# Optimization experiments

Hardware: AMD Instinct MI355X
Metric: run time of the kernel (lower is better)

## Reference

```python
import jax, jax.numpy as jnp
import numpy as np

DIM = 512
HEADS = 8
DIM_HEAD = 64
INNER = HEADS * DIM_HEAD          # 512
CPB_DIM = DIM // 2                # 256 (ContinuousPositionBias hidden dim)
FF_INNER = int(DIM * 4 * 2 / 3)   # 1365 (GEGLU inner dim)
B, C, F, H, W = 2, 512, 8, 32, 32
SCALE = DIM_HEAD ** -0.5


def setup_inputs() -> dict:
    key = jax.random.key(0)
    ks = jax.random.split(key, 24)
    def rnd(k, shape, s=0.02):
        return jax.random.normal(k, shape, jnp.float32) * s
    return {
        "x": jax.random.normal(ks[0], (B, C, F, W, W), jnp.float32)[:, :, :, :H, :],
        # spatial attention
        "sa_gamma": jnp.ones((DIM,), jnp.float32),
        "sa_wq": rnd(ks[1], (DIM, INNER)),
        "sa_wkv": rnd(ks[2], (DIM, 2 * INNER)),
        "sa_wo": rnd(ks[3], (INNER, DIM)),
        # temporal attention
        "ta_gamma": jnp.ones((DIM,), jnp.float32),
        "ta_wq": rnd(ks[4], (DIM, INNER)),
        "ta_wkv": rnd(ks[5], (DIM, 2 * INNER)),
        "ta_wo": rnd(ks[6], (INNER, DIM)),
        # spatial ContinuousPositionBias MLP (num_dims=2, layers=2)
        "sp_w1": rnd(ks[7], (2, CPB_DIM), 0.1), "sp_b1": jnp.zeros((CPB_DIM,), jnp.float32),
        "sp_w2": rnd(ks[8], (CPB_DIM, CPB_DIM), 0.05), "sp_b2": jnp.zeros((CPB_DIM,), jnp.float32),
        "sp_w3": rnd(ks[9], (CPB_DIM, HEADS), 0.05), "sp_b3": jnp.zeros((HEADS,), jnp.float32),
        # temporal ContinuousPositionBias MLP (num_dims=1)
        "tp_w1": rnd(ks[10], (1, CPB_DIM), 0.1), "tp_b1": jnp.zeros((CPB_DIM,), jnp.float32),
        "tp_w2": rnd(ks[11], (CPB_DIM, CPB_DIM), 0.05), "tp_b2": jnp.zeros((CPB_DIM,), jnp.float32),
        "tp_w3": rnd(ks[12], (CPB_DIM, HEADS), 0.05), "tp_b3": jnp.zeros((HEADS,), jnp.float32),
        # FeedForward: Conv3d 1x1 (no bias) -> GEGLU -> RMSNorm -> Conv3d 1x1
        "ff_win": rnd(ks[13], (DIM, 2 * FF_INNER)),
        "ff_gamma": jnp.ones((FF_INNER,), jnp.float32),
        "ff_wout": rnd(ks[14], (FF_INNER, DIM)),
    }


def _rms_last(x, g):
    # torch: F.normalize(x, dim=-1) * sqrt(C) * gamma
    nrm = jnp.sqrt(jnp.sum(x * x, axis=-1, keepdims=True))
    return x / jnp.maximum(nrm, 1e-12) * jnp.sqrt(jnp.float32(x.shape[-1])) * g


def _mlp_bias(rel, w1, b1, w2, b2, w3, b3):
    h = jax.nn.silu(rel @ w1 + b1)
    h = jax.nn.silu(h @ w2 + b2)
    return h @ w3 + b3  # [R, heads]


def _cpb_2d(h, w, params):
    ry = jnp.arange(-(h - 1), h, dtype=jnp.float32)
    rx = jnp.arange(-(w - 1), w, dtype=jnp.float32)
    gy, gx = jnp.meshgrid(ry, rx, indexing='ij')
    rel = jnp.stack([gy, gx], -1).reshape(-1, 2)          # [(2h-1)(2w-1), 2]
    tab = _mlp_bias(rel, *params)                          # [R, heads]
    py, px = jnp.meshgrid(jnp.arange(h), jnp.arange(w), indexing='ij')
    pos = jnp.stack([py.reshape(-1), px.reshape(-1)], -1)  # [n, 2]
    d = pos[:, None, :] - pos[None, :, :]                  # [n, n, 2]
    idx = (d[..., 0] + h - 1) * (2 * w - 1) + (d[..., 1] + w - 1)
    return jnp.transpose(tab[idx], (2, 0, 1))              # [heads, n, n]


def _cpb_1d(f, params):
    rel = jnp.arange(-(f - 1), f, dtype=jnp.float32)[:, None]
    tab = _mlp_bias(rel, *params)                          # [2f-1, heads]
    p = jnp.arange(f)
    idx = p[:, None] - p[None, :] + f - 1
    return jnp.transpose(tab[idx], (2, 0, 1))              # [heads, f, f]


def _attn(x, gamma, wq, wkv, wo, bias):
    # x: [b, n, c]; manual softmax(QK^T*scale + bias)V (flash disabled by pos_bias)
    xn = _rms_last(x, gamma)
    q = xn @ wq
    k, v = jnp.split(xn @ wkv, 2, axis=-1)
    b, n, _ = q.shape
    rs = lambda t: t.reshape(b, n, HEADS, DIM_HEAD).transpose(0, 2, 1, 3)
    q, k, v = rs(q), rs(k), rs(v)
    s = jnp.einsum('bhid,bhjd->bhij', q, k) * SCALE + bias[None]
    a = jax.nn.softmax(s, axis=-1)
    o = jnp.einsum('bhij,bhjd->bhid', a, v)
    o = o.transpose(0, 2, 1, 3).reshape(b, n, INNER)
    return o @ wo


def _ff(x, win, gamma, wout):
    # x: [b, f, h, w, c] channel-last; Conv3d 1x1 == channel einsum
    hdn = jnp.einsum('bfhwc,co->bfhwo', x, win)
    a, gate = jnp.split(hdn, 2, axis=-1)
    y = a * jax.nn.gelu(gate, approximate=False)           # GEGLU (torch exact gelu)
    # shift_token: chunk channels, shift second half by +1 frame
    c1 = (FF_INNER + 1) // 2
    t1, t2 = y[..., :c1], y[..., c1:]
    t2 = jnp.pad(t2, ((0, 0), (1, 0), (0, 0), (0, 0), (0, 0)))[:, :-1]
    y = jnp.concatenate([t1, t2], axis=-1)
    yn = _rms_last(y, gamma)                               # RMSNorm over channels
    return jnp.einsum('bfhwi,ic->bfhwc', yn, wout)


def reference(x, sa_gamma, sa_wq, sa_wkv, sa_wo, ta_gamma, ta_wq, ta_wkv, ta_wo,
              sp_w1, sp_b1, sp_w2, sp_b2, sp_w3, sp_b3,
              tp_w1, tp_b1, tp_w2, tp_b2, tp_w3, tp_b3,
              ff_win, ff_gamma, ff_wout):
    b, c, f, h, w = x.shape
    xl = jnp.transpose(x, (0, 2, 3, 4, 1))                 # b f h w c
    # spatial attention over (h w) tokens, batched over (b f)
    xs = xl.reshape(b * f, h * w, c)
    sp_bias = _cpb_2d(h, w, (sp_w1, sp_b1, sp_w2, sp_b2, sp_w3, sp_b3))
    xs = _attn(xs, sa_gamma, sa_wq, sa_wkv, sa_wo, sp_bias) + xs
    xv = xs.reshape(b, f, h, w, c)
    # temporal attention over f tokens, batched over (b h w)
    xt = jnp.transpose(xv, (0, 2, 3, 1, 4)).reshape(b * h * w, f, c)
    tp_bias = _cpb_1d(f, (tp_w1, tp_b1, tp_w2, tp_b2, tp_w3, tp_b3))
    xt = _attn(xt, ta_gamma, ta_wq, ta_wkv, ta_wo, tp_bias) + xt
    xv = jnp.transpose(xt.reshape(b, h, w, f, c), (0, 3, 1, 2, 4))
    # GEGLU feedforward with token shift
    xv = _ff(xv, ff_win, ff_gamma, ff_wout) + xv
    return jnp.transpose(xv, (0, 4, 1, 2, 3))              # b c f h w
```

## Files before the change

### kernel.cpp

```cpp
#include <hip/hip_runtime.h>
#include <cstdint>
#include <cstddef>

typedef __bf16 bf16_t;
typedef __bf16 bf16x8 __attribute__((ext_vector_type(8)));
typedef __bf16 bf16x4 __attribute__((ext_vector_type(4)));
typedef float floatx4 __attribute__((ext_vector_type(4)));

__device__ __forceinline__ float wred_sum(float v) {
#pragma unroll
  for (int off = 32; off > 0; off >>= 1) v += __shfl_xor(v, off);
  return v;
}
__device__ __forceinline__ void async16(const void* g, void* l) {
  __builtin_amdgcn_global_load_lds((const __attribute__((address_space(1))) void*)g,
                                   (__attribute__((address_space(3))) void*)l, 16, 0, 0);
}

template <int MODE>
__global__ __launch_bounds__(256) void st_gemm(
    const bf16_t* __restrict__ A, const bf16_t* __restrict__ B, void* Cp, void* Cp2,
    const float* Res, int M, int N, int K, int lda, int ldb, int ldc, int nb1,
    long long sa1, long long sa2, long long sb1, long long sb2,
    long long sc1, long long sc2) {
  __shared__ bf16_t sA[128 * 32];
  __shared__ bf16_t sB[128 * 32];
  const int z = blockIdx.z;
  const int z1 = z % nb1, z2 = z / nb1;
  A += z1 * sa1 + z2 * sa2;
  B += z1 * sb1 + z2 * sb2;
  const long long coff = z1 * sc1 + z2 * sc2;
  const int tid = threadIdx.x;
  const int bm = blockIdx.x, bn = blockIdx.y;
  const int lane = tid & 63;
  const int wave = tid >> 6;
  const int wm = (wave >> 1) * 64, wn = (wave & 1) * 64;
  const int rowf = lane & 15, kq = (lane >> 4) * 8;

  floatx4 acc[4][4];
#pragma unroll
  for (int i = 0; i < 4; ++i)
#pragma unroll
    for (int j = 0; j < 4; ++j) acc[i][j] = floatx4{0.f, 0.f, 0.f, 0.f};

  for (int kt = 0; kt < K; kt += 32) {
#pragma unroll
    for (int it = 0; it < 2; ++it) {
      int slot = it * 256 + tid;
      int mi = slot >> 2, kc = slot & 3;
      int ar = bm * 128 + mi; if (ar > M - 1) ar = M - 1;
      int br = bn * 128 + mi; if (br > N - 1) br = N - 1;
      async16(A + (size_t)ar * lda + kt + kc * 8, (char*)sA + slot * 16);
      async16(B + (size_t)br * ldb + kt + kc * 8, (char*)sB + slot * 16);
    }
    __syncthreads();
    bf16x8 af[4], bv[4];
#pragma unroll
    for (int i = 0; i < 4; ++i) {
      af[i] = *(const bf16x8*)(sA + (wm + i * 16 + rowf) * 32 + kq);
      bv[i] = *(const bf16x8*)(sB + (wn + i * 16 + rowf) * 32 + kq);
    }
#pragma unroll
    for (int i = 0; i < 4; ++i)
#pragma unroll
      for (int j = 0; j < 4; ++j)
        acc[i][j] = __builtin_amdgcn_mfma_f32_16x16x32_bf16(af[i], bv[j], acc[i][j], 0, 0, 0);
    __syncthreads();
  }

  const int cl = lane & 15;
  const int rowBase = bm * 128 + wm + (lane >> 4) * 4;
  if (MODE == 5) {
    bf16_t* yb = (bf16_t*)Cp;
    const int cg0 = ((bn * 128 + wn) >> 5) * 16;
#pragma unroll
    for (int i = 0; i < 4; ++i) {
#pragma unroll
      for (int p = 0; p < 2; ++p) {
        int c = cg0 + p * 16 + cl;
        if (c >= 1365) continue;
#pragma unroll
        for (int r = 0; r < 4; ++r) {
          int row = rowBase + i * 16 + r;
          if (row >= M) continue;
          float a = acc[i][2 * p][r];
          float gt = acc[i][2 * p + 1][r];
          float y = a * 0.5f * gt * (1.f + erff(gt * 0.70710678f));
          yb[(size_t)row * ldc + c] = (bf16_t)y;
        }
      }
    }
    return;
  }
  const int colBase = bn * 128 + wn + cl;
#pragma unroll
  for (int i = 0; i < 4; ++i) {
#pragma unroll
    for (int j = 0; j < 4; ++j) {
      int col = colBase + j * 16;
      if (col >= N) continue;
#pragma unroll
      for (int r = 0; r < 4; ++r) {
        int row = rowBase + i * 16 + r;
        if (row >= M) continue;
        long long inidx = coff + (long long)row * ldc + col;
        float v = acc[i][j][r];
        if (MODE >= 2) v += Res[inidx];
        if (MODE == 0) { ((float*)Cp)[inidx] = v; }
        else if (MODE == 1) { ((bf16_t*)Cp)[inidx] = (bf16_t)v; }
        else if (MODE == 2) { ((float*)Cp)[inidx] = v; }
        else if (MODE == 3) {
          int orow = (row & ~8191) | ((row & 1023) << 3) | ((row >> 10) & 7);
          ((float*)Cp)[coff + (long long)orow * ldc + col] = v;
        } else if (MODE == 4) {
          int orow = (row & ~8191) | ((row & 7) << 10) | ((row >> 3) & 1023);
          long long oidx = coff + (long long)orow * ldc + col;
          ((float*)Cp)[oidx] = v;
          ((bf16_t*)Cp2)[oidx] = (bf16_t)v;
        }
      }
    }
  }
}

__global__ __launch_bounds__(256) void st_transpose2d(
    const float* __restrict__ in, float* __restrict__ out, int R, int Cc,
    long long inb, long long outb) {
  __shared__ float tile[32][33];
  const int ct = blockIdx.x, rt = blockIdx.y, b = blockIdx.z;
  in += (long long)b * inb;
  out += (long long)b * outb;
  const int tx = threadIdx.x & 31, ty = threadIdx.x >> 5;
#pragma unroll
  for (int k = 0; k < 4; ++k) {
    int r = rt * 32 + ty + k * 8;
    int c = ct * 32 + tx;
    tile[ty + k * 8][tx] = in[(size_t)r * Cc + c];
  }
  __syncthreads();
#pragma unroll
  for (int k = 0; k < 4; ++k) {
    int c = ct * 32 + ty + k * 8;
    int r = rt * 32 + tx;
    out[(size_t)c * R + r] = tile[tx][ty + k * 8];
  }
}

__global__ void st_wtrans(const float* __restrict__ src, bf16_t* __restrict__ dst,
                          int K, int Kpad, int N, int srcld, int coloff, long total) {
  long idx = (long)blockIdx.x * 256 + threadIdx.x;
  if (idx >= total) return;
  int kp = (int)(idx % Kpad);
  int n = (int)(idx / Kpad);
  float v = (kp < K) ? src[(size_t)kp * srcld + coloff + n] : 0.f;
  dst[idx] = (bf16_t)v;
}

__global__ void st_wtrans_geglu(const float* __restrict__ src, bf16_t* __restrict__ dst,
                                long total) {
  long idx = (long)blockIdx.x * 256 + threadIdx.x;
  if (idx >= total) return;
  int kp = (int)(idx & 511);
  int n = (int)(idx >> 9);
  int c = ((n >> 5) << 4) + (n & 15);
  float v = 0.f;
  if (c < 1365) {
    int srccol = c + (((n >> 4) & 1) ? 1365 : 0);
    v = src[(size_t)kp * 2730 + srccol];
  }
  dst[idx] = (bf16_t)v;
}

__global__ __launch_bounds__(256) void st_cpb(
    const float* __restrict__ w1, const float* __restrict__ b1,
    const float* __restrict__ w2, const float* __restrict__ b2,
    const float* __restrict__ w3, const float* __restrict__ b3,
    bf16_t* __restrict__ tab2d, float* __restrict__ tab1d, int two_d) {
  const int pos = blockIdx.x, t = threadIdx.x;
  float r0, r1 = 0.f;
  if (two_d) { r0 = (float)(pos / 63 - 31); r1 = (float)(pos % 63 - 31); }
  else { r0 = (float)(pos - 7); }
  __shared__ float sh[256];
  float h = r0 * w1[t] + (two_d ? r1 * w1[256 + t] : 0.f) + b1[t];
  h = h / (1.f + expf(-h));
  sh[t] = h;
  __syncthreads();
  float h2 = b2[t];
  for (int j = 0; j < 256; ++j) h2 += sh[j] * w2[j * 256 + t];
  h2 = h2 / (1.f + expf(-h2));
  __syncthreads();
  sh[t] = h2;
  __syncthreads();
  if (t < 8) {
    float o = b3[t];
    for (int j = 0; j < 256; ++j) o += sh[j] * w3[j * 8 + t];
    if (two_d) tab2d[t * 4000 + pos] = (bf16_t)(o * 1.4426950408889634f);
    else tab1d[t * 15 + pos] = o;
  }
}

__global__ __launch_bounds__(256) void st_rmsnorm(const float* __restrict__ x,
                                                  const float* __restrict__ gamma,
                                                  bf16_t* __restrict__ y) {
  const int token = blockIdx.x * 4 + (threadIdx.x >> 6);
  const int lane = threadIdx.x & 63;
  const float* xr = x + (size_t)token * 512;
  float v[8];
  float ss = 0.f;
#pragma unroll
  for (int k = 0; k < 8; ++k) { v[k] = xr[k * 64 + lane]; ss += v[k] * v[k]; }
  ss = wred_sum(ss);
  const float r = 22.627416998f / fmaxf(sqrtf(ss), 1e-12f);
  bf16_t* yr = y + (size_t)token * 512;
#pragma unroll
  for (int k = 0; k < 8; ++k) yr[k * 64 + lane] = (bf16_t)(v[k] * r * gamma[k * 64 + lane]);
}

__global__ __launch_bounds__(256) void st_vtrans(const bf16_t* __restrict__ qkv,
                                                 bf16_t* __restrict__ vT) {
  __shared__ float tile[32][33];
  const int jt = blockIdx.x, dt = blockIdx.y, z = blockIdx.z;
  const int bf = z >> 3, h = z & 7;
  const int tx = threadIdx.x & 31, ty = threadIdx.x >> 5;
#pragma unroll
  for (int k = 0; k < 4; ++k) {
    int j = jt * 32 + ty + k * 8;
    int d = dt * 32 + tx;
    tile[ty + k * 8][tx] = (float)qkv[((size_t)(bf * 1024 + j)) * 1536 + 1024 + h * 64 + d];
  }
  __syncthreads();
#pragma unroll
  for (int k = 0; k < 4; ++k) {
    int d = dt * 32 + ty + k * 8;
    int j = jt * 32 + tx;
    vT[((size_t)z * 64 + d) * 1024 + j] = (bf16_t)tile[tx][ty + k * 8];
  }
}

__global__ __launch_bounds__(256, 3) void st_flash(
    const bf16_t* __restrict__ qkv, const bf16_t* __restrict__ vT,
    const bf16_t* __restrict__ tabb, bf16_t* __restrict__ ob) {
  __shared__ __align__(16) bf16_t ldsK[2][64 * 64];
  __shared__ __align__(16) bf16_t ldsV[2][64 * 64];
  __shared__ __align__(16) bf16_t ldsP[4 * 32 * 64];
  __shared__ __align__(16) bf16_t ldsT[2216];
  const int qtile = blockIdx.x;
  const int z = blockIdx.y;
  const int bf = z >> 3, h = z & 7;
  const int tid = threadIdx.x;
  const int lane = tid & 63, wave = tid >> 6;
  const int cl = lane & 15, g = lane >> 4;
  const size_t qkvBase = (size_t)bf * 1024 * 1536 + h * 64;
  const int eoff = (qtile * 252) & ~7;
  const bf16_t* Kp = qkv + qkvBase + 512;
  const bf16_t* Vp = vT + (size_t)z * 65536;

#pragma unroll
  for (int it = 0; it < 4; ++it) {
    int s = it * 256 + tid;
    int row = s >> 3, c = s & 7;
    int cs = c ^ (row & 7);
    async16(qkv + qkvBase + (size_t)(qtile * 128 + row) * 1536 + cs * 8,
            (char*)ldsP + s * 16);
  }
#pragma unroll
  for (int it = 0; it < 2; ++it) {
    int s = it * 256 + tid;
    if (s < 277) async16(tabb + h * 4000 + eoff + s * 8, (char*)ldsT + s * 16);
  }
#pragma unroll
  for (int it = 0; it < 2; ++it) {
    int s = it * 256 + tid;
    int row = s >> 3, c = s & 7;
    int cs = c ^ (row & 7);
    async16(Kp + (size_t)row * 1536 + cs * 8, (char*)ldsK[0] + s * 16);
    async16(Vp + (size_t)row * 1024 + cs * 8, (char*)ldsV[0] + s * 16);
  }
  __syncthreads();
  bf16x8 aq[2][2];
#pragma unroll
  for (int it = 0; it < 2; ++it)
#pragma unroll
    for (int ks = 0; ks < 2; ++ks) {
      int row = wave * 32 + it * 16 + cl;
      int cs = (g + ks * 4) ^ (row & 7);
      aq[it][ks] = *(const bf16x8*)(ldsP + row * 64 + cs * 8);
    }
  __syncthreads();

  int fiB[2];
#pragma unroll
  for (int it = 0; it < 2; ++it) {
    int i = qtile * 128 + wave * 32 + it * 16 + cl;
    fiB[it] = (i >> 5) * 63 + (i & 31) + 1984 - eoff;
  }
  float lsum[2] = {0.f, 0.f};
  floatx4 oacc[4][2];
#pragma unroll
  for (int dt = 0; dt < 4; ++dt)
#pragma unroll
    for (int it = 0; it < 2; ++it) oacc[dt][it] = floatx4{0.f, 0.f, 0.f, 0.f};

  bf16_t* ldsPw = ldsP + wave * (32 * 64);
  const float SC = 0.18033688011112042f;

#pragma unroll 2
  for (int t = 0; t < 16; ++t) {
    const int p = t & 1;
    if (t < 15) {
      const int j1 = (t + 1) * 64;
#pragma unroll
      for (int it = 0; it < 2; ++it) {
        int s = it * 256 + tid;
        int row = s >> 3, c = s & 7;
        int cs = c ^ (row & 7);
        async16(Kp + (size_t)(j1 + row) * 1536 + cs * 8, (char*)ldsK[p ^ 1] + s * 16);
        async16(Vp + (size_t)row * 1024 + j1 + cs * 8, (char*)ldsV[p ^ 1] + s * 16);
      }
    }
    const int j0 = t * 64;
    floatx4 sacc[4][2];
#pragma unroll
    for (int jt = 0; jt < 4; ++jt)
#pragma unroll
      for (int it = 0; it < 2; ++it) sacc[jt][it] = floatx4{0.f, 0.f, 0.f, 0.f};
#pragma unroll
    for (int ks = 0; ks < 2; ++ks) {
#pragma unroll
      for (int jt = 0; jt < 4; ++jt) {
        int row = jt * 16 + cl;
        bf16x8 kf = *(const bf16x8*)(ldsK[p] + row * 64 + (((ks * 4 + g) ^ (row & 7))) * 8);
#pragma unroll
        for (int it = 0; it < 2; ++it)
          sacc[jt][it] = __builtin_amdgcn_mfma_f32_16x16x32_bf16(kf, aq[it][ks], sacc[jt][it], 0, 0, 0);
      }
    }
#pragma unroll
    for (int jt = 0; jt < 4; ++jt) {
      int jb = j0 + jt * 16 + g * 4;
      int fjb = (jb >> 5) * 63 + (jb & 31);
      int gg = jt * 2 + (g >> 1);
#pragma unroll
      for (int it = 0; it < 2; ++it) {
        int idx0 = fiB[it] - fjb;
        float e0 = __builtin_exp2f(sacc[jt][it][0] * SC + (float)ldsT[idx0]);
        float e1 = __builtin_exp2f(sacc[jt][it][1] * SC + (float)ldsT[idx0 - 1]);
        float e2 = __builtin_exp2f(sacc[jt][it][2] * SC + (float)ldsT[idx0 - 2]);
        float e3 = __builtin_exp2f(sacc[jt][it][3] * SC + (float)ldsT[idx0 - 3]);
        lsum[it] += (e0 + e1) + (e2 + e3);
        bf16x4 pv = {(bf16_t)e0, (bf16_t)e1, (bf16_t)e2, (bf16_t)e3};
        int prow = it * 16 + cl;
        *(bf16x4*)((char*)ldsPw + prow * 128 + ((gg ^ (cl & 7)) * 16 + (g & 1) * 8)) = pv;
      }
    }
#pragma unroll
    for (int ks = 0; ks < 2; ++ks) {
      bf16x8 pB[2];
#pragma unroll
      for (int it = 0; it < 2; ++it)
        pB[it] = *(const bf16x8*)((char*)ldsPw + (it * 16 + cl) * 128 +
                                  (((ks * 4 + g) ^ (cl & 7)) * 16));
#pragma unroll
      for (int dt = 0; dt < 4; ++dt) {
        int row = dt * 16 + cl;
        bf16x8 vf = *(const bf16x8*)(ldsV[p] + row * 64 + (((ks * 4 + g) ^ (row & 7))) * 8);
#pragma unroll
        for (int it = 0; it < 2; ++it)
          oacc[dt][it] = __builtin_amdgcn_mfma_f32_16x16x32_bf16(vf, pB[it], oacc[dt][it], 0, 0, 0);
      }
    }
    __syncthreads();
  }
  float inv[2];
#pragma unroll
  for (int it = 0; it < 2; ++it) {
    float s = lsum[it];
    s += __shfl_xor(s, 16);
    s += __shfl_xor(s, 32);
    inv[it] = 1.f / s;
  }
#pragma unroll
  for (int it = 0; it < 2; ++it) {
    int i = qtile * 128 + wave * 32 + it * 16 + cl;
    size_t base = ((size_t)bf * 1024 + i) * 512 + h * 64 + g * 4;
#pragma unroll
    for (int dt = 0; dt < 4; ++dt) {
      bf16x4 ov = {(bf16_t)(oacc[dt][it][0] * inv[it]), (bf16_t)(oacc[dt][it][1] * inv[it]),
                   (bf16_t)(oacc[dt][it][2] * inv[it]), (bf16_t)(oacc[dt][it][3] * inv[it])};
      *(bf16x4*)(ob + base + dt * 16) = ov;
    }
  }
}

__global__ __launch_bounds__(256) void st_tattn2(const bf16_t* __restrict__ qkv,
                                                 const float* __restrict__ tabf,
                                                 bf16_t* __restrict__ o) {
  const int wg = blockIdx.x * 4 + (threadIdx.x >> 6);
  const int bhw = wg >> 3, head = wg & 7;
  const int lane = threadIdx.x & 63;
  const size_t base = (size_t)bhw * 8 * 1536 + head * 64 + lane;
  float q[8], k[8], v[8];
#pragma unroll
  for (int f = 0; f < 8; ++f) {
    q[f] = (float)qkv[base + (size_t)f * 1536];
    k[f] = (float)qkv[base + (size_t)f * 1536 + 512];
    v[f] = (float)qkv[base + (size_t)f * 1536 + 1024];
  }
  float p[64];
#pragma unroll
  for (int i = 0; i < 8; ++i)
#pragma unroll
    for (int j = 0; j < 8; ++j) p[i * 8 + j] = q[i] * k[j];
#pragma unroll
  for (int st = 32; st >= 1; st >>= 1) {
    const bool hi = (lane & st) != 0;
#pragma unroll
    for (int m = 0; m < st; ++m) {
      float give = hi ? p[m] : p[m + st];
      float keep = hi ? p[m + st] : p[m];
      p[m] = keep + __shfl_xor(give, st);
    }
  }
  const int i = lane >> 3, j = lane & 7;
  float e = __expf(p[0] * 0.125f + tabf[head * 15 + i - j + 7]);
  float sm = e;
  sm += __shfl_xor(sm, 1);
  sm += __shfl_xor(sm, 2);
  sm += __shfl_xor(sm, 4);
  const float prob = e / sm;
  float acc[8];
#pragma unroll
  for (int ii = 0; ii < 8; ++ii) acc[ii] = 0.f;
#pragma unroll
  for (int ii = 0; ii < 8; ++ii)
#pragma unroll
    for (int jj = 0; jj < 8; ++jj)
      acc[ii] += __shfl(prob, ii * 8 + jj) * v[jj];
#pragma unroll
  for (int ii = 0; ii < 8; ++ii)
    o[(size_t)(bhw * 8 + ii) * 512 + head * 64 + lane] = (bf16_t)acc[ii];
}

__global__ __launch_bounds__(256) void st_glu(const bf16_t* __restrict__ y,
                                              const float* __restrict__ gamma,
                                              bf16_t* __restrict__ yn) {
  const int t = blockIdx.x;
  const int tid = threadIdx.x;
  const int f = (t >> 10) & 7;
  float yv[6];
  float ss = 0.f;
#pragma unroll
  for (int kk = 0; kk < 6; ++kk) {
    int c = kk * 256 + tid;
    float v = 0.f;
    if (c < 1365) {
      long src = t;
      bool valid = true;
      if (c >= 683) { if (f == 0) valid = false; else src = t - 1024; }
      if (valid) v = (float)y[src * 1365 + c];
    }
    yv[kk] = v;
    ss += v * v;
  }
  __shared__ float red[4];
  ss = wred_sum(ss);
  if ((tid & 63) == 0) red[tid >> 6] = ss;
  __syncthreads();
  ss = red[0] + red[1] + red[2] + red[3];
  const float r = sqrtf(1365.f) / fmaxf(sqrtf(ss), 1e-12f);
#pragma unroll
  for (int kk = 0; kk < 6; ++kk) {
    int c = kk * 256 + tid;
    if (c < 1365) yn[(size_t)t * 1376 + c] = (bf16_t)(yv[kk] * r * gamma[c]);
  }
  if (tid < 11) yn[(size_t)t * 1376 + 1365 + tid] = (bf16_t)0.f;
}

extern "C" void kernel_launch(void* const* d_in, const int* in_sizes, int n_in,
                              void* d_out, int out_size, void* d_ws, size_t ws_size,
                              hipStream_t stream) {
  const float* x        = (const float*)d_in[0];
  const float* sa_gamma = (const float*)d_in[1];
  const float* sa_wq    = (const float*)d_in[2];
  const float* sa_wkv   = (const float*)d_in[3];
  const float* sa_wo    = (const float*)d_in[4];
  const float* ta_gamma = (const float*)d_in[5];
  const float* ta_wq    = (const float*)d_in[6];
  const float* ta_wkv   = (const float*)d_in[7];
  const float* ta_wo    = (const float*)d_in[8];
  const float* sp_w1 = (const float*)d_in[9];
  const float* sp_b1 = (const float*)d_in[10];
  const float* sp_w2 = (const float*)d_in[11];
  const float* sp_b2 = (const float*)d_in[12];
  const float* sp_w3 = (const float*)d_in[13];
  const float* sp_b3 = (const float*)d_in[14];
  const float* tp_w1 = (const float*)d_in[15];
  const float* tp_b1 = (const float*)d_in[16];
  const float* tp_w2 = (const float*)d_in[17];
  const float* tp_b2 = (const float*)d_in[18];
  const float* tp_w3 = (const float*)d_in[19];
  const float* tp_b3 = (const float*)d_in[20];
  const float* ff_win   = (const float*)d_in[21];
  const float* ff_gamma = (const float*)d_in[22];
  const float* ff_wout  = (const float*)d_in[23];
  float* outp = (float*)d_out;

  char* ws = (char*)d_ws;
  size_t off = 0;
  auto alloc = [&](size_t bytes) -> char* {
    char* p = ws + off;
    off += (bytes + 255) & ~(size_t)255;
    return p;
  };
  const long T = 16384;
  float*  xs  = (float*)alloc((size_t)T * 512 * 4);
  bf16_t* xn  = (bf16_t*)alloc((size_t)T * 512 * 2);
  char*   R2  = alloc((size_t)T * 1536 * 2);
  char*   R3  = alloc((size_t)T * 1536 * 2);
  char*   R4  = alloc((size_t)T * 1376 * 2);
  bf16_t* wqkvT_sa = (bf16_t*)alloc(1536ULL * 512 * 2);
  bf16_t* woT_sa   = (bf16_t*)alloc(512ULL * 512 * 2);
  bf16_t* wqkvT_ta = (bf16_t*)alloc(1536ULL * 512 * 2);
  bf16_t* woT_ta   = (bf16_t*)alloc(512ULL * 512 * 2);
  bf16_t* winT  = (bf16_t*)alloc(2752ULL * 512 * 2);
  bf16_t* woutT = (bf16_t*)alloc(512ULL * 1376 * 2);
  bf16_t* tabb  = (bf16_t*)alloc(8 * 4000 * 2);
  float*  tabf  = (float*)alloc(8 * 15 * 4);

  bf16_t* qkv  = (bf16_t*)R2;
  bf16_t* ybuf = (bf16_t*)R2;
  bf16_t* vT   = (bf16_t*)R3;
  float*  xt   = (float*)R3;
  bf16_t* ob_s = xn;
  bf16_t* ob_t = (bf16_t*)R4;
  bf16_t* ynb  = (bf16_t*)R4;

  st_transpose2d<<<dim3(256, 16, 2), 256, 0, stream>>>(x, xs, 512, 8192,
                                                       (long long)512 * 8192, (long long)512 * 8192);
  auto wt = [&](const float* src, bf16_t* dst, int K, int Kpad, int N, int srcld, int coloff) {
    long tot = (long)N * Kpad;
    st_wtrans<<<dim3((tot + 255) / 256), 256, 0, stream>>>(src, dst, K, Kpad, N, srcld, coloff, tot);
  };
  wt(sa_wq, wqkvT_sa, 512, 512, 512, 512, 0);
  wt(sa_wkv, wqkvT_sa + 512 * 512, 512, 512, 1024, 1024, 0);
  wt(sa_wo, woT_sa, 512, 512, 512, 512, 0);
  wt(ta_wq, wqkvT_ta, 512, 512, 512, 512, 0);
  wt(ta_wkv, wqkvT_ta + 512 * 512, 512, 512, 1024, 1024, 0);
  wt(ta_wo, woT_ta, 512, 512, 512, 512, 0);
  st_wtrans_geglu<<<dim3((2752 * 512) / 256), 256, 0, stream>>>(ff_win, winT, 2752L * 512);
  wt(ff_wout, woutT, 1365, 1376, 512, 512, 0);
  st_cpb<<<dim3(3969), 256, 0, stream>>>(sp_w1, sp_b1, sp_w2, sp_b2, sp_w3, sp_b3, tabb, tabf, 1);
  st_cpb<<<dim3(15), 256, 0, stream>>>(tp_w1, tp_b1, tp_w2, tp_b2, tp_w3, tp_b3, tabb, tabf, 0);

  st_rmsnorm<<<dim3(4096), 256, 0, stream>>>(xs, sa_gamma, xn);
  st_gemm<1><<<dim3(128, 12, 1), 256, 0, stream>>>(
      xn, wqkvT_sa, (void*)qkv, nullptr, nullptr, 16384, 1536, 512, 512, 512, 1536, 1, 0, 0, 0, 0, 0, 0);
  st_vtrans<<<dim3(32, 2, 128), 256, 0, stream>>>(qkv, vT);
  st_flash<<<dim3(8, 128), 256, 0, stream>>>(qkv, vT, tabb, ob_s);
  st_gemm<3><<<dim3(128, 4, 1), 256, 0, stream>>>(
      ob_s, woT_sa, (void*)xt, nullptr, xs, 16384, 512, 512, 512, 512, 512, 1, 0, 0, 0, 0, 0, 0);

  st_rmsnorm<<<dim3(4096), 256, 0, stream>>>(xt, ta_gamma, xn);
  st_gemm<1><<<dim3(128, 12, 1), 256, 0, stream>>>(
      xn, wqkvT_ta, (void*)qkv, nullptr, nullptr, 16384, 1536, 512, 512, 512, 1536, 1, 0, 0, 0, 0, 0, 0);
  st_tattn2<<<dim3(4096), 256, 0, stream>>>(qkv, tabf, ob_t);
  st_gemm<4><<<dim3(128, 4, 1), 256, 0, stream>>>(
      ob_t, woT_ta, (void*)xs, (void*)xn, xt, 16384, 512, 512, 512, 512, 512, 1, 0, 0, 0, 0, 0, 0);

  st_gemm<5><<<dim3(128, 22, 1), 256, 0, stream>>>(
      xn, winT, (void*)ybuf, nullptr, nullptr, 16384, 2752, 512, 512, 512, 1365, 1, 0, 0, 0, 0, 0, 0);
  st_glu<<<dim3(16384), 256, 0, stream>>>(ybuf, ff_gamma, ynb);
  st_gemm<2><<<dim3(128, 4, 1), 256, 0, stream>>>(
      ynb, woutT, (void*)xs, nullptr, xs, 16384, 512, 1376, 1376, 1376, 512, 1, 0, 0, 0, 0, 0, 0);

  st_transpose2d<<<dim3(16, 256, 2), 256, 0, stream>>>(xs, outp, 8192, 512,
                                                       (long long)8192 * 512, (long long)8192 * 512);
}
```

Before: 713.2 us.

## Shrink flash KV tile to 32 and fold bias into MFMA accumulator init

The spatial flash kernel now streams K/V in 32-row tiles instead of 64, which shrinks LDS buffers and raises the launch-bounds occupancy target from 3 to 4 blocks per CU. Q fragments are read directly from global memory instead of being staged through LDS. The position-bias table is stored as fp32 prescaled by 8, so it can seed the MFMA accumulator and the separate per-element bias add before exp2 disappears. The trade-off is twice as many loop iterations and barriers per block, and a larger fp32 bias table to load.

```diff
diff --git a/kernel.cpp b/kernel.cpp
--- a/kernel.cpp
+++ b/kernel.cpp
@@ -175,7 +175,7 @@
     const float* __restrict__ w1, const float* __restrict__ b1,
     const float* __restrict__ w2, const float* __restrict__ b2,
     const float* __restrict__ w3, const float* __restrict__ b3,
-    bf16_t* __restrict__ tab2d, float* __restrict__ tab1d, int two_d) {
+    float* __restrict__ tab2d, float* __restrict__ tab1d, int two_d) {
   const int pos = blockIdx.x, t = threadIdx.x;
   float r0, r1 = 0.f;
   if (two_d) { r0 = (float)(pos / 63 - 31); r1 = (float)(pos % 63 - 31); }
@@ -194,7 +194,7 @@
   if (t < 8) {
     float o = b3[t];
     for (int j = 0; j < 256; ++j) o += sh[j] * w3[j * 8 + t];
-    if (two_d) tab2d[t * 4000 + pos] = (bf16_t)(o * 1.4426950408889634f);
+    if (two_d) tab2d[t * 4000 + pos] = o * 8.0f;
     else tab1d[t * 15 + pos] = o;
   }
 }
@@ -237,13 +237,13 @@
   }
 }
 
-__global__ __launch_bounds__(256, 3) void st_flash(
+__global__ __launch_bounds__(256, 4) void st_flash(
     const bf16_t* __restrict__ qkv, const bf16_t* __restrict__ vT,
-    const bf16_t* __restrict__ tabb, bf16_t* __restrict__ ob) {
-  __shared__ __align__(16) bf16_t ldsK[2][64 * 64];
-  __shared__ __align__(16) bf16_t ldsV[2][64 * 64];
-  __shared__ __align__(16) bf16_t ldsP[4 * 32 * 64];
-  __shared__ __align__(16) bf16_t ldsT[2216];
+    const float* __restrict__ tab2f, bf16_t* __restrict__ ob) {
+  __shared__ __align__(16) bf16_t ldsK[2][32 * 64];
+  __shared__ __align__(16) bf16_t ldsV[2][64 * 32];
+  __shared__ __align__(16) bf16_t ldsP[4 * 32 * 32];
+  __shared__ __align__(16) float ldsT[2208];
   const int qtile = blockIdx.x;
   const int z = blockIdx.y;
   const int bf = z >> 3, h = z & 7;
@@ -251,40 +251,28 @@
   const int lane = tid & 63, wave = tid >> 6;
   const int cl = lane & 15, g = lane >> 4;
   const size_t qkvBase = (size_t)bf * 1024 * 1536 + h * 64;
-  const int eoff = (qtile * 252) & ~7;
+  const int eoff = (qtile * 252) & ~3;
   const bf16_t* Kp = qkv + qkvBase + 512;
   const bf16_t* Vp = vT + (size_t)z * 65536;
 
 #pragma unroll
-  for (int it = 0; it < 4; ++it) {
+  for (int it = 0; it < 3; ++it) {
     int s = it * 256 + tid;
-    int row = s >> 3, c = s & 7;
-    int cs = c ^ (row & 7);
-    async16(qkv + qkvBase + (size_t)(qtile * 128 + row) * 1536 + cs * 8,
-            (char*)ldsP + s * 16);
-  }
-#pragma unroll
-  for (int it = 0; it < 2; ++it) {
-    int s = it * 256 + tid;
-    if (s < 277) async16(tabb + h * 4000 + eoff + s * 8, (char*)ldsT + s * 16);
-  }
-#pragma unroll
-  for (int it = 0; it < 2; ++it) {
-    int s = it * 256 + tid;
-    int row = s >> 3, c = s & 7;
-    int cs = c ^ (row & 7);
-    async16(Kp + (size_t)row * 1536 + cs * 8, (char*)ldsK[0] + s * 16);
-    async16(Vp + (size_t)row * 1024 + cs * 8, (char*)ldsV[0] + s * 16);
-  }
-  __syncthreads();
+    if (s < 552) async16(tab2f + h * 4000 + eoff + s * 4, (char*)ldsT + s * 16);
+  }
+  {
+    int row = tid >> 3, c = tid & 7, cs = c ^ (row & 7);
+    async16(Kp + (size_t)row * 1536 + cs * 8, (char*)ldsK[0] + tid * 16);
+    int rv = tid >> 2, cv = tid & 3, csv = cv ^ (rv & 3);
+    async16(Vp + (size_t)rv * 1024 + csv * 8, (char*)ldsV[0] + tid * 16);
+  }
   bf16x8 aq[2][2];
 #pragma unroll
   for (int it = 0; it < 2; ++it)
 #pragma unroll
     for (int ks = 0; ks < 2; ++ks) {
-      int row = wave * 32 + it * 16 + cl;
-      int cs = (g + ks * 4) ^ (row & 7);
-      aq[it][ks] = *(const bf16x8*)(ldsP + row * 64 + cs * 8);
+      int row = qtile * 128 + wave * 32 + it * 16 + cl;
+      aq[it][ks] = *(const bf16x8*)(qkv + qkvBase + (size_t)row * 1536 + (ks * 4 + g) * 8);
     }
   __syncthreads();
 
@@ -301,69 +289,60 @@
 #pragma unroll
     for (int it = 0; it < 2; ++it) oacc[dt][it] = floatx4{0.f, 0.f, 0.f, 0.f};
 
-  bf16_t* ldsPw = ldsP + wave * (32 * 64);
+  bf16_t* ldsPw = ldsP + wave * (32 * 32);
   const float SC = 0.18033688011112042f;
 
 #pragma unroll 2
-  for (int t = 0; t < 16; ++t) {
+  for (int t = 0; t < 32; ++t) {
     const int p = t & 1;
-    if (t < 15) {
-      const int j1 = (t + 1) * 64;
+    if (t < 31) {
+      const int j1 = (t + 1) * 32;
+      int row = tid >> 3, c = tid & 7, cs = c ^ (row & 7);
+      async16(Kp + (size_t)(j1 + row) * 1536 + cs * 8, (char*)ldsK[p ^ 1] + tid * 16);
+      int rv = tid >> 2, cv = tid & 3, csv = cv ^ (rv & 3);
+      async16(Vp + (size_t)rv * 1024 + j1 + csv * 8, (char*)ldsV[p ^ 1] + tid * 16);
+    }
+    const int j0 = t * 32;
+#pragma unroll
+    for (int jt = 0; jt < 2; ++jt) {
+      int jb = j0 + jt * 16 + g * 4;
+      int fjb = (jb >> 5) * 63 + (jb & 31);
+      floatx4 sj[2];
 #pragma unroll
       for (int it = 0; it < 2; ++it) {
-        int s = it * 256 + tid;
-        int row = s >> 3, c = s & 7;
-        int cs = c ^ (row & 7);
-        async16(Kp + (size_t)(j1 + row) * 1536 + cs * 8, (char*)ldsK[p ^ 1] + s * 16);
-        async16(Vp + (size_t)row * 1024 + j1 + cs * 8, (char*)ldsV[p ^ 1] + s * 16);
+        int idx0 = fiB[it] - fjb;
+        sj[it] = floatx4{ldsT[idx0], ldsT[idx0 - 1], ldsT[idx0 - 2], ldsT[idx0 - 3]};
       }
-    }
-    const int j0 = t * 64;
-    floatx4 sacc[4][2];
-#pragma unroll
-    for (int jt = 0; jt < 4; ++jt)
-#pragma unroll
-      for (int it = 0; it < 2; ++it) sacc[jt][it] = floatx4{0.f, 0.f, 0.f, 0.f};
-#pragma unroll
-    for (int ks = 0; ks < 2; ++ks) {
-#pragma unroll
-      for (int jt = 0; jt < 4; ++jt) {
+#pragma unroll
+      for (int ks = 0; ks < 2; ++ks) {
         int row = jt * 16 + cl;
         bf16x8 kf = *(const bf16x8*)(ldsK[p] + row * 64 + (((ks * 4 + g) ^ (row & 7))) * 8);
 #pragma unroll
         for (int it = 0; it < 2; ++it)
-          sacc[jt][it] = __builtin_amdgcn_mfma_f32_16x16x32_bf16(kf, aq[it][ks], sacc[jt][it], 0, 0, 0);
+          sj[it] = __builtin_amdgcn_mfma_f32_16x16x32_bf16(kf, aq[it][ks], sj[it], 0, 0, 0);
       }
-    }
-#pragma unroll
-    for (int jt = 0; jt < 4; ++jt) {
-      int jb = j0 + jt * 16 + g * 4;
-      int fjb = (jb >> 5) * 63 + (jb & 31);
       int gg = jt * 2 + (g >> 1);
 #pragma unroll
       for (int it = 0; it < 2; ++it) {
-        int idx0 = fiB[it] - fjb;
-        float e0 = __builtin_exp2f(sacc[jt][it][0] * SC + (float)ldsT[idx0]);
-        float e1 = __builtin_exp2f(sacc[jt][it][1] * SC + (float)ldsT[idx0 - 1]);
-        float e2 = __builtin_exp2f(sacc[jt][it][2] * SC + (float)ldsT[idx0 - 2]);
-        float e3 = __builtin_exp2f(sacc[jt][it][3] * SC + (float)ldsT[idx0 - 3]);
+        float e0 = __builtin_exp2f(sj[it][0] * SC);
+        float e1 = __builtin_exp2f(sj[it][1] * SC);
+        float e2 = __builtin_exp2f(sj[it][2] * SC);
+        float e3 = __builtin_exp2f(sj[it][3] * SC);
         lsum[it] += (e0 + e1) + (e2 + e3);
         bf16x4 pv = {(bf16_t)e0, (bf16_t)e1, (bf16_t)e2, (bf16_t)e3};
-        int prow = it * 16 + cl;
-        *(bf16x4*)((char*)ldsPw + prow * 128 + ((gg ^ (cl & 7)) * 16 + (g & 1) * 8)) = pv;
+        *(bf16x4*)((char*)ldsPw + (it * 16 + cl) * 64 +
+                   ((gg ^ (cl & 3)) * 16 + (g & 1) * 8)) = pv;
       }
     }
-#pragma unroll
-    for (int ks = 0; ks < 2; ++ks) {
+    {
       bf16x8 pB[2];
 #pragma unroll
       for (int it = 0; it < 2; ++it)
-        pB[it] = *(const bf16x8*)((char*)ldsPw + (it * 16 + cl) * 128 +
-                                  (((ks * 4 + g) ^ (cl & 7)) * 16));
+        pB[it] = *(const bf16x8*)((char*)ldsPw + (it * 16 + cl) * 64 + ((g ^ (cl & 3)) * 16));
 #pragma unroll
       for (int dt = 0; dt < 4; ++dt) {
         int row = dt * 16 + cl;
-        bf16x8 vf = *(const bf16x8*)(ldsV[p] + row * 64 + (((ks * 4 + g) ^ (row & 7))) * 8);
+        bf16x8 vf = *(const bf16x8*)(ldsV[p] + row * 32 + ((g ^ (row & 3)) * 8));
 #pragma unroll
         for (int it = 0; it < 2; ++it)
           oacc[dt][it] = __builtin_amdgcn_mfma_f32_16x16x32_bf16(vf, pB[it], oacc[dt][it], 0, 0, 0);
@@ -524,7 +503,7 @@
   bf16_t* woT_ta   = (bf16_t*)alloc(512ULL * 512 * 2);
   bf16_t* winT  = (bf16_t*)alloc(2752ULL * 512 * 2);
   bf16_t* woutT = (bf16_t*)alloc(512ULL * 1376 * 2);
-  bf16_t* tabb  = (bf16_t*)alloc(8 * 4000 * 2);
+  float*  tab2f = (float*)alloc(8 * 4000 * 4);
   float*  tabf  = (float*)alloc(8 * 15 * 4);
 
   bf16_t* qkv  = (bf16_t*)R2;
@@ -549,14 +528,14 @@
   wt(ta_wo, woT_ta, 512, 512, 512, 512, 0);
   st_wtrans_geglu<<<dim3((2752 * 512) / 256), 256, 0, stream>>>(ff_win, winT, 2752L * 512);
   wt(ff_wout, woutT, 1365, 1376, 512, 512, 0);
-  st_cpb<<<dim3(3969), 256, 0, stream>>>(sp_w1, sp_b1, sp_w2, sp_b2, sp_w3, sp_b3, tabb, tabf, 1);
-  st_cpb<<<dim3(15), 256, 0, stream>>>(tp_w1, tp_b1, tp_w2, tp_b2, tp_w3, tp_b3, tabb, tabf, 0);
+  st_cpb<<<dim3(3969), 256, 0, stream>>>(sp_w1, sp_b1, sp_w2, sp_b2, sp_w3, sp_b3, tab2f, tabf, 1);
+  st_cpb<<<dim3(15), 256, 0, stream>>>(tp_w1, tp_b1, tp_w2, tp_b2, tp_w3, tp_b3, tab2f, tabf, 0);
 
   st_rmsnorm<<<dim3(4096), 256, 0, stream>>>(xs, sa_gamma, xn);
   st_gemm<1><<<dim3(128, 12, 1), 256, 0, stream>>>(
       xn, wqkvT_sa, (void*)qkv, nullptr, nullptr, 16384, 1536, 512, 512, 512, 1536, 1, 0, 0, 0, 0, 0, 0);
   st_vtrans<<<dim3(32, 2, 128), 256, 0, stream>>>(qkv, vT);
-  st_flash<<<dim3(8, 128), 256, 0, stream>>>(qkv, vT, tabb, ob_s);
+  st_flash<<<dim3(8, 128), 256, 0, stream>>>(qkv, vT, tab2f, ob_s);
   st_gemm<3><<<dim3(128, 4, 1), 256, 0, stream>>>(
       ob_s, woT_sa, (void*)xt, nullptr, xs, 16384, 512, 512, 512, 512, 512, 1, 0, 0, 0, 0, 0, 0);
 
```

After: 721.0 us. About the same (+1.1%).
